# Kernel tuning notes

Measured on AMD Instinct MI355X. Metric: run time of the kernel, lower is better.

The kernel has to match this reference:

```python
import jax, jax.numpy as jnp
import numpy as np

T, B, SEQ_WIDTH, HID = 512, 64, 64, 1024
N = 32  # sqrt(HID): associative memory is N x N, HID spiking neurons
BETA = 0.9     # leak
THRESH = 1.0   # firing threshold
SLOPE = 25.0   # fast-sigmoid surrogate slope (snntorch default)


@jax.custom_vjp
def spike(u):
    # Heaviside forward, fast-sigmoid surrogate backward (snntorch-style)
    return (u > 0).astype(u.dtype)

def _spike_fwd(u):
    return (u > 0).astype(u.dtype), u

def _spike_bwd(u, g):
    sg = 1.0 / (1.0 + SLOPE * jnp.abs(u)) ** 2
    return (g * sg,)

spike.defvjp(_spike_fwd, _spike_bwd)


def assoc_leaky(h, Wk, bk, Wv, bv, Wq, bq):
    """Leaky associative spiking layer.
    h: (T, B, HID). Membrane state is an (B, N, N) associative matrix.
    Each step: outer-product write of key/value, leaky integration,
    threshold spike with soft reset, output spikes gated by sigmoid(q) rows.
    """
    k = h @ Wk + bk                      # (T, B, N)
    v = h @ Wv + bv                      # (T, B, N)
    q = jax.nn.sigmoid(h @ Wq + bq)      # (T, B, N)  use_q_projection gate
    Bt = h.shape[1]

    def step(mem, kvq):
        kt, vt, qt = kvq
        mem = BETA * mem + kt[:, :, None] * vt[:, None, :]   # (B, N, N)
        s = spike(mem - THRESH)
        mem = mem - s * THRESH                               # soft reset
        out = (s * qt[:, :, None]).reshape(Bt, N * N)        # (B, HID)
        return mem, out

    mem0 = jnp.zeros((Bt, N, N), h.dtype)
    _, outs = jax.lax.scan(step, mem0, (k, v, q))
    return outs  # (T, B, HID)


def setup_inputs() -> dict:
    key = jax.random.key(0)
    ks = jax.random.split(key, 12)
    s = 0.02
    def p(k, shape):
        return jax.random.normal(k, shape, jnp.float32) * s
    z = lambda *shape: jnp.zeros(shape, jnp.float32)
    return {
        "x": jax.random.normal(ks[0], (T, B, SEQ_WIDTH + 1), jnp.float32),
        "W_in": p(ks[1], (SEQ_WIDTH + 1, HID)), "b_in": z(HID),
        "Wk1": p(ks[2], (HID, N)), "bk1": z(N),
        "Wv1": p(ks[3], (HID, N)), "bv1": z(N),
        "Wq1": p(ks[4], (HID, N)), "bq1": z(N),
        "W_mid": p(ks[5], (HID, HID)), "b_mid": z(HID),
        "Wk2": p(ks[6], (HID, N)), "bk2": z(N),
        "Wv2": p(ks[7], (HID, N)), "bv2": z(N),
        "Wq2": p(ks[8], (HID, N)), "bq2": z(N),
        "W_out": p(ks[9], (HID, SEQ_WIDTH)), "b_out": z(SEQ_WIDTH),
    }


def reference(x, W_in, b_in, Wk1, bk1, Wv1, bv1, Wq1, bq1,
              W_mid, b_mid, Wk2, bk2, Wv2, bv2, Wq2, bq2, W_out, b_out):
    h = x @ W_in + b_in                                  # (T, B, HID)
    h = assoc_leaky(h, Wk1, bk1, Wv1, bv1, Wq1, bq1)
    h = jax.nn.relu(h @ W_mid + b_mid)
    h = assoc_leaky(h, Wk2, bk2, Wv2, bv2, Wq2, bq2)
    y = h @ W_out + b_out                                # (T, B, SEQ_WIDTH)
    return jax.nn.sigmoid(y)
```

## Files before the change

### kernel.cpp

```cpp
#include <hip/hip_runtime.h>
#include <math.h>


#define T_STEPS 512
#define BATCH   64
#define NN      32
#define HID     1024
#define INW     65
#define OUTW    64
#define KVQ     96

__device__ __forceinline__ float sigmoidf_(float x) { return 1.0f / (1.0f + expf(-x)); }

__global__ __launch_bounds__(512) void prep_kernel(
    const float* __restrict__ W_in, const float* __restrict__ b_in,
    const float* __restrict__ Wk1, const float* __restrict__ bk1,
    const float* __restrict__ Wv1, const float* __restrict__ bv1,
    const float* __restrict__ Wq1, const float* __restrict__ bq1,
    const float* __restrict__ b_mid,
    const float* __restrict__ Wk2, const float* __restrict__ bk2,
    const float* __restrict__ Wv2, const float* __restrict__ bv2,
    const float* __restrict__ Wq2, const float* __restrict__ bq2,
    float* __restrict__ W1eff, float* __restrict__ b1eff,
    float* __restrict__ const2)
{
    const int m = blockIdx.x;
    const int tid = threadIdx.x;
    __shared__ float srcv[HID];
    __shared__ float part[512];
    for (int h = tid; h < HID; h += 512) {
        float s;
        if (m < INW)       s = W_in[m * HID + h];
        else if (m == INW) s = b_in[h];
        else               s = fmaxf(b_mid[h], 0.f);
        srcv[h] = s;
    }
    __syncthreads();
    const int hq = tid >> 7, ns = tid & 127;
    const int sel = ns >> 5, nn = ns & 31;
    const bool layer2 = (m == INW + 1);
    const float* W = layer2 ? (sel == 0 ? Wk2 : sel == 1 ? Wv2 : Wq2)
                            : (sel == 0 ? Wk1 : sel == 1 ? Wv1 : Wq1);
    float acc = 0.f;
    if (ns < KVQ) {
        const int h0 = hq * 256;
        #pragma unroll 8
        for (int hh = 0; hh < 256; ++hh)
            acc = fmaf(srcv[h0 + hh], W[(h0 + hh) * NN + nn], acc);
    }
    part[tid] = acc;
    __syncthreads();
    if (hq == 0 && ns < KVQ) {
        float tot = part[ns] + part[128 + ns] + part[256 + ns] + part[384 + ns];
        if (m < INW) {
            W1eff[m * KVQ + ns] = tot;
        } else if (m == INW) {
            tot += (sel == 0 ? bk1 : sel == 1 ? bv1 : bq1)[nn];
            b1eff[ns] = tot;
        } else {
            tot += (sel == 0 ? bk2 : sel == 1 ? bv2 : bq2)[nn];
            const2[ns] = (sel == 2) ? sigmoidf_(tot) : tot;
        }
    }
}

__global__ __launch_bounds__(128) void kvq1p1_kernel(
    const float* __restrict__ x, const float* __restrict__ W1eff,
    const float* __restrict__ b1eff, float* __restrict__ kvq1,
    float* __restrict__ S, float* __restrict__ P)
{
    const int b = blockIdx.x >> 3, seg = blockIdx.x & 7;
    const int tid = threadIdx.x;
    __shared__ __align__(16) float Ws[INW * KVQ];
    __shared__ __align__(16) float bs[KVQ];
    __shared__ __align__(16) float pool[64 * 100];
    for (int i4 = tid; i4 < (INW * KVQ) / 4; i4 += 128)
        ((float4*)Ws)[i4] = ((const float4*)W1eff)[i4];
    if (tid < KVQ) bs[tid] = b1eff[tid];
    for (int l = tid; l < 64 * INW; l += 128) {
        const int r = l / INW, m = l - r * INW;
        pool[m * 68 + r] = x[((size_t)((seg * 64 + r) * 64 + b)) * INW + m];
    }
    __syncthreads();
    const int rg = tid >> 3;
    const int c0 = (tid & 7) * 12;
    float acc[4][12];
    #pragma unroll
    for (int r = 0; r < 4; ++r)
        #pragma unroll
        for (int k = 0; k < 12; ++k) acc[r][k] = bs[c0 + k];
    #pragma unroll 5
    for (int m = 0; m < INW; ++m) {
        const float4 xv = *(const float4*)&pool[m * 68 + rg * 4];
        const float4 w0 = *(const float4*)&Ws[m * KVQ + c0];
        const float4 w1 = *(const float4*)&Ws[m * KVQ + c0 + 4];
        const float4 w2 = *(const float4*)&Ws[m * KVQ + c0 + 8];
        const float xr[4] = {xv.x, xv.y, xv.z, xv.w};
        const float wk[12] = {w0.x, w0.y, w0.z, w0.w, w1.x, w1.y, w1.z, w1.w,
                              w2.x, w2.y, w2.z, w2.w};
        #pragma unroll
        for (int r = 0; r < 4; ++r)
            #pragma unroll
            for (int k = 0; k < 12; ++k)
                acc[r][k] = fmaf(xr[r], wk[k], acc[r][k]);
    }
    __syncthreads();
    #pragma unroll
    for (int r = 0; r < 4; ++r) {
        const int row = rg * 4 + r;
        float v[12];
        #pragma unroll
        for (int k = 0; k < 12; ++k)
            v[k] = (c0 + k >= 2 * NN) ? sigmoidf_(acc[r][k]) : acc[r][k];
        float* kt = &pool[row * 100 + c0];
        *(float4*)&kt[0] = make_float4(v[0], v[1], v[2], v[3]);
        *(float4*)&kt[4] = make_float4(v[4], v[5], v[6], v[7]);
        *(float4*)&kt[8] = make_float4(v[8], v[9], v[10], v[11]);
        float* o = kvq1 + ((size_t)b * T_STEPS + seg * 64 + row) * KVQ + c0;
        *(float4*)&o[0] = make_float4(v[0], v[1], v[2], v[3]);
        *(float4*)&o[4] = make_float4(v[4], v[5], v[6], v[7]);
        *(float4*)&o[8] = make_float4(v[8], v[9], v[10], v[11]);
    }
    __syncthreads();
    const int i0 = (tid >> 5) * 8, j = tid & 31;
    float p[8], am[8];
    #pragma unroll
    for (int r = 0; r < 8; ++r) { p[r] = 0.f; am[r] = 0.f; }
    for (int tt = 0; tt < 16; ++tt) {
        float4 k0[4], k1[4]; float vv[4];
        #pragma unroll
        for (int d2 = 0; d2 < 4; ++d2) {
            const int t = tt * 4 + d2;
            k0[d2] = *(const float4*)&pool[t * 100 + i0];
            k1[d2] = *(const float4*)&pool[t * 100 + i0 + 4];
            vv[d2] = pool[t * 100 + 32 + j];
        }
        #pragma unroll
        for (int d2 = 0; d2 < 4; ++d2) {
            const float kf[8] = {k0[d2].x, k0[d2].y, k0[d2].z, k0[d2].w,
                                 k1[d2].x, k1[d2].y, k1[d2].z, k1[d2].w};
            #pragma unroll
            for (int r = 0; r < 8; ++r) {
                p[r] = fmaf(0.9f, p[r], kf[r] * vv[d2]);
                am[r] = fmaxf(am[r], fabsf(p[r]));
            }
        }
    }
    const size_t o = ((size_t)seg * 64 + b) * 1024;
    #pragma unroll
    for (int r = 0; r < 8; ++r) {
        S[o + (i0 + r) * 32 + j] = p[r];
        P[o + (i0 + r) * 32 + j] = am[r];
    }
}

__global__ __launch_bounds__(256) void cc_kernel(
    const float* __restrict__ S, const float* __restrict__ P,
    const float* __restrict__ kvq,
    unsigned int* __restrict__ rowany, unsigned int* __restrict__ dmask)
{
    const int b = blockIdx.x;
    const int tid = threadIdx.x;
    const float c64 = 0.0011790184577738599f;
    float M[4] = {0.f, 0.f, 0.f, 0.f};
    bool fl = false;
    #pragma unroll
    for (int g = 0; g < 8; ++g) {
        #pragma unroll
        for (int k = 0; k < 4; ++k) {
            const size_t o = (size_t)g * 65536 + (size_t)b * 1024 + k * 256 + tid;
            const float s = S[o], pm = P[o];
            const float ub = fmaxf(M[k], 0.f) + pm;
            fl |= !(ub * 1.0001f <= 0.999f);
            M[k] = fmaf(c64, M[k], s);
        }
    }
    __shared__ unsigned int flr[4];
    const unsigned long long bal = __ballot(fl);
    if ((tid & 63) == 0) flr[tid >> 6] = (bal != 0ULL) ? 1u : 0u;
    __syncthreads();
    if ((flr[0] | flr[1] | flr[2] | flr[3]) == 0u) {
        if (tid < 64) rowany[b * 64 + tid] = 0u;
        return;
    }
    __shared__ float buf[64 * 64];
    const int j = tid & 31, ig = tid >> 5;
    const int wavei = tid >> 6;
    float mem[4] = {0.f, 0.f, 0.f, 0.f};
    unsigned int u[4] = {0u, 0u, 0u, 0u};
    for (int c = 0; c < 8; ++c) {
        __syncthreads();
        #pragma unroll
        for (int r = 0; r < 4; ++r) {
            const int s4 = tid + 256 * r;
            const int dt = s4 >> 4, q = s4 & 15;
            *(float4*)&buf[dt * 64 + q * 4] =
                *(const float4*)(kvq + ((size_t)b * T_STEPS + c * 64 + dt) * KVQ + q * 4);
        }
        __syncthreads();
        for (int dt = 0; dt < 64; ++dt) {
            const float4 kk = *(const float4*)&buf[dt * 64 + ig * 4];
            const float vv = buf[dt * 64 + 32 + j];
            const float kf[4] = {kk.x, kk.y, kk.z, kk.w};
            #pragma unroll
            for (int r = 0; r < 4; ++r) {
                mem[r] = fmaf(0.9f, mem[r], kf[r] * vv);
                const bool s = mem[r] > 1.f; if (s) mem[r] -= 1.f;
                u[r] |= (s ? 1u : 0u) << (dt & 31);
            }
            if ((dt & 31) == 31) {
                const int wg = c * 2 + (dt >> 5);
                unsigned int* dm = dmask + (size_t)(wg * 64 + b) * 1024;
                unsigned int a = 0;
                #pragma unroll
                for (int r = 0; r < 4; ++r) {
                    dm[(ig * 4 + r) * 32 + j] = u[r];
                    a |= u[r]; u[r] = 0u;
                }
                #pragma unroll
                for (int off = 32; off; off >>= 1) a |= __shfl_xor(a, off);
                if ((tid & 63) == 0) rowany[(b * 4 + wavei) * 16 + wg] = a;
            }
        }
    }
}

__global__ __launch_bounds__(128) void midp1_kernel(
    const unsigned int* __restrict__ rowany1, const unsigned int* __restrict__ dmask1,
    const float* __restrict__ kvq1,
    const float* __restrict__ W_mid, const float* __restrict__ b_mid,
    const float* __restrict__ Wk2, const float* __restrict__ bk2,
    const float* __restrict__ Wv2, const float* __restrict__ bv2,
    const float* __restrict__ Wq2, const float* __restrict__ bq2,
    const float* __restrict__ const2, float* __restrict__ kvq2,
    float* __restrict__ S2, float* __restrict__ P2)
{
    const int b = blockIdx.x >> 3, seg = blockIdx.x & 7;
    const int tid = threadIdx.x;
    const int w0 = seg * 2;
    const unsigned int orA = rowany1[(b * 4 + 0) * 16 + w0] | rowany1[(b * 4 + 1) * 16 + w0]
                           | rowany1[(b * 4 + 2) * 16 + w0] | rowany1[(b * 4 + 3) * 16 + w0];
    const unsigned int orB = rowany1[(b * 4 + 0) * 16 + w0 + 1] | rowany1[(b * 4 + 1) * 16 + w0 + 1]
                           | rowany1[(b * 4 + 2) * 16 + w0 + 1] | rowany1[(b * 4 + 3) * 16 + w0 + 1];
    __shared__ __align__(16) float c2s[KVQ];
    if (tid < KVQ) c2s[tid] = const2[tid];
    __syncthreads();
    float* obase = kvq2 + ((size_t)b * T_STEPS + seg * 64) * KVQ;
    const size_t o2 = ((size_t)seg * 64 + b) * 1024;
    const int i0 = (tid >> 5) * 8, j = tid & 31;
    const float G64 = 9.988209815422261f;
    if ((orA | orB) == 0u) {
        for (int l = tid; l < 64 * 24; l += 128) {
            const int row = l / 24, c4 = l - row * 24;
            *(float4*)&obase[row * KVQ + c4 * 4] = ((const float4*)c2s)[c4];
        }
        #pragma unroll
        for (int r = 0; r < 8; ++r) {
            const float s = c2s[i0 + r] * c2s[32 + j] * G64;
            S2[o2 + (i0 + r) * 32 + j] = s;
            P2[o2 + (i0 + r) * 32 + j] = fabsf(s);
        }
        return;
    }
    __shared__ __align__(16) float kt2[64 * 64];
    __shared__ float h2[HID];
    __shared__ unsigned int msk[NN];
    for (int d = 0; d < 64; ++d) {
        const unsigned int orw = (d < 32) ? orA : orB;
        const int bit = d & 31;
        if (!((orw >> bit) & 1u)) {
            if (tid < 16) *(float4*)&kt2[d * 64 + tid * 4] = ((const float4*)c2s)[tid];
            if (tid < 24) *(float4*)&obase[d * KVQ + tid * 4] = ((const float4*)c2s)[tid];
        } else {
            const int wg = w0 + (d >> 5);
            const unsigned int* dmw = dmask1 + (size_t)(wg * 64 + b) * 1024;
            for (int i2 = 0; i2 < NN; i2 += 4) {
                const int i = i2 + (tid >> 5);
                const unsigned int wb = dmw[i * 32 + (tid & 31)];
                const unsigned long long balm = __ballot(((wb >> bit) & 1u) != 0);
                const int ibase = i2 + (tid >> 6) * 2;
                if ((tid & 63) == 0)  msk[ibase]     = (unsigned int)balm;
                if ((tid & 63) == 32) msk[ibase + 1] = (unsigned int)(balm >> 32);
            }
            for (int cc = tid; cc < HID; cc += 128) h2[cc] = b_mid[cc];
            __syncthreads();
            const float* qrow = kvq1 + ((size_t)b * T_STEPS + seg * 64 + d) * KVQ + 2 * NN;
            for (int i = 0; i < NN; ++i) {
                unsigned int m = msk[i];
                if (!m) continue;
                const float qv = qrow[i];
                while (m) {
                    const int jj = __ffs(m) - 1; m &= m - 1;
                    const float* wr = W_mid + (size_t)(i * NN + jj) * HID;
                    for (int cc = tid; cc < HID; cc += 128)
                        h2[cc] = fmaf(qv, wr[cc], h2[cc]);
                }
            }
            __syncthreads();
            for (int cc = tid; cc < HID; cc += 128) h2[cc] = fmaxf(h2[cc], 0.f);
            __syncthreads();
            if (tid < KVQ) {
                const int sel = tid >> 5, nn = tid & 31;
                const float* W2 = sel == 0 ? Wk2 : sel == 1 ? Wv2 : Wq2;
                float a2 = (sel == 0 ? bk2 : sel == 1 ? bv2 : bq2)[nn];
                for (int cc = 0; cc < HID; ++cc)
                    a2 = fmaf(h2[cc], W2[cc * NN + nn], a2);
                if (sel == 2) a2 = sigmoidf_(a2);
                obase[d * KVQ + tid] = a2;
                if (tid < 64) kt2[d * 64 + tid] = a2;
            }
            __syncthreads();
        }
    }
    __syncthreads();
    float p[8], am[8];
    #pragma unroll
    for (int r = 0; r < 8; ++r) { p[r] = 0.f; am[r] = 0.f; }
    for (int tt = 0; tt < 16; ++tt) {
        float4 k0[4], k1[4]; float vv[4];
        #pragma unroll
        for (int d2 = 0; d2 < 4; ++d2) {
            const int t = tt * 4 + d2;
            k0[d2] = *(const float4*)&kt2[t * 64 + i0];
            k1[d2] = *(const float4*)&kt2[t * 64 + i0 + 4];
            vv[d2] = kt2[t * 64 + 32 + j];
        }
        #pragma unroll
        for (int d2 = 0; d2 < 4; ++d2) {
            const float kf[8] = {k0[d2].x, k0[d2].y, k0[d2].z, k0[d2].w,
                                 k1[d2].x, k1[d2].y, k1[d2].z, k1[d2].w};
            #pragma unroll
            for (int r = 0; r < 8; ++r) {
                p[r] = fmaf(0.9f, p[r], kf[r] * vv[d2]);
                am[r] = fmaxf(am[r], fabsf(p[r]));
            }
        }
    }
    #pragma unroll
    for (int r = 0; r < 8; ++r) {
        S2[o2 + (i0 + r) * 32 + j] = p[r];
        P2[o2 + (i0 + r) * 32 + j] = am[r];
    }
}

__global__ __launch_bounds__(256) void out_kernel(
    const unsigned int* __restrict__ rowany2, const unsigned int* __restrict__ dmask2,
    const float* __restrict__ kvq2,
    const float* __restrict__ W_out, const float* __restrict__ b_out,
    float* __restrict__ y)
{
    const int blk = blockIdx.x;
    const int b = blk >> 2, tq = blk & 3;
    const int tid = threadIdx.x;
    const int wave = tid >> 6, lane = tid & 63;
    const int wg = tq * 4 + wave;
    __shared__ unsigned int mskws[4][NN];
    const int g16 = lane & 15;
    const float4 bo = ((const float4*)b_out)[g16];
    const float4 sy = make_float4(sigmoidf_(bo.x), sigmoidf_(bo.y),
                                  sigmoidf_(bo.z), sigmoidf_(bo.w));
    const unsigned int or4 = rowany2[(b * 4 + 0) * 16 + wg]
                           | rowany2[(b * 4 + 1) * 16 + wg]
                           | rowany2[(b * 4 + 2) * 16 + wg]
                           | rowany2[(b * 4 + 3) * 16 + wg];
    if (or4 == 0) {
        #pragma unroll
        for (int d = 0; d < 32; d += 4) {
            const int t = wg * 32 + d + (lane >> 4);
            ((float4*)(y + ((size_t)t * 64 + b) * OUTW))[g16] = sy;
        }
        return;
    }
    for (int d = 0; d < 32; ++d) {
        const int t = wg * 32 + d;
        float* yr = y + ((size_t)t * 64 + b) * OUTW;
        if (!((or4 >> d) & 1u)) {
            if (lane < 16) ((float4*)yr)[lane] = sy;
            continue;
        }
        const unsigned int* dmw = dmask2 + (size_t)(wg * 64 + b) * 1024;
        for (int i2 = 0; i2 < NN; i2 += 2) {
            const int i = i2 + (lane >> 5), jj = lane & 31;
            const unsigned int wbits = dmw[i * 32 + jj];
            const unsigned long long bal = __ballot(((wbits >> d) & 1u) != 0);
            if (lane == 0)  mskws[wave][i2] = (unsigned int)bal;
            if (lane == 32) mskws[wave][i2 + 1] = (unsigned int)(bal >> 32);
        }
        const float* qrow = kvq2 + ((size_t)b * T_STEPS + t) * KVQ + 2 * NN;
        float a = b_out[lane];
        for (int i = 0; i < NN; ++i) {
            unsigned int m = mskws[wave][i];
            if (!m) continue;
            const float qv = qrow[i];
            while (m) {
                const int jj = __ffs(m) - 1; m &= m - 1;
                a = fmaf(qv, W_out[(size_t)(i * NN + jj) * OUTW + lane], a);
            }
        }
        yr[lane] = sigmoidf_(a);
    }
}

extern "C" void kernel_launch(void* const* d_in, const int* in_sizes, int n_in,
                              void* d_out, int out_size, void* d_ws, size_t ws_size,
                              hipStream_t stream)
{
    const float* x     = (const float*)d_in[0];
    const float* W_in  = (const float*)d_in[1];
    const float* b_in  = (const float*)d_in[2];
    const float* Wk1   = (const float*)d_in[3];
    const float* bk1   = (const float*)d_in[4];
    const float* Wv1   = (const float*)d_in[5];
    const float* bv1   = (const float*)d_in[6];
    const float* Wq1   = (const float*)d_in[7];
    const float* bq1   = (const float*)d_in[8];
    const float* W_mid = (const float*)d_in[9];
    const float* b_mid = (const float*)d_in[10];
    const float* Wk2   = (const float*)d_in[11];
    const float* bk2   = (const float*)d_in[12];
    const float* Wv2   = (const float*)d_in[13];
    const float* bv2   = (const float*)d_in[14];
    const float* Wq2   = (const float*)d_in[15];
    const float* bq2   = (const float*)d_in[16];
    const float* W_out = (const float*)d_in[17];
    const float* b_out = (const float*)d_in[18];
    float* y = (float*)d_out;

    float* ws = (float*)d_ws;
    float* W1eff  = ws;
    float* b1eff  = ws + 6240;
    float* const2 = ws + 6336;
    float* kvq1   = ws + 8192;
    float* kvq2   = kvq1 + 3145728;
    unsigned int* dmask1  = (unsigned int*)(kvq2 + 3145728);
    unsigned int* dmask2  = dmask1 + 1048576;
    unsigned int* rowany1 = dmask2 + 1048576;
    unsigned int* rowany2 = rowany1 + 4096;
    float* S1 = (float*)(rowany2 + 4096);
    float* P1 = S1 + 524288;
    float* S2 = P1 + 524288;
    float* P2 = S2 + 524288;

    prep_kernel<<<INW + 2, 512, 0, stream>>>(W_in, b_in, Wk1, bk1, Wv1, bv1, Wq1, bq1,
                                             b_mid, Wk2, bk2, Wv2, bv2, Wq2, bq2,
                                             W1eff, b1eff, const2);
    kvq1p1_kernel<<<BATCH * 8, 128, 0, stream>>>(x, W1eff, b1eff, kvq1, S1, P1);
    cc_kernel<<<BATCH, 256, 0, stream>>>(S1, P1, kvq1, rowany1, dmask1);
    midp1_kernel<<<BATCH * 8, 128, 0, stream>>>(rowany1, dmask1, kvq1, W_mid, b_mid,
                                                Wk2, bk2, Wv2, bv2, Wq2, bq2,
                                                const2, kvq2, S2, P2);
    cc_kernel<<<BATCH, 256, 0, stream>>>(S2, P2, kvq2, rowany2, dmask2);
    out_kernel<<<BATCH * 4, 256, 0, stream>>>(rowany2, dmask2, kvq2, W_out, b_out, y);
}
```

Measured before the change: 151.9 us.

## Replace per-element spike certificates with per-block max bounds and skip constant segments

```diff
diff --git a/kernel.cpp b/kernel.cpp
--- a/kernel.cpp
+++ b/kernel.cpp
@@ -67,13 +67,14 @@
 __global__ __launch_bounds__(128) void kvq1p1_kernel(
     const float* __restrict__ x, const float* __restrict__ W1eff,
     const float* __restrict__ b1eff, float* __restrict__ kvq1,
-    float* __restrict__ S, float* __restrict__ P)
+    float* __restrict__ cert1)
 {
     const int b = blockIdx.x >> 3, seg = blockIdx.x & 7;
     const int tid = threadIdx.x;
     __shared__ __align__(16) float Ws[INW * KVQ];
     __shared__ __align__(16) float bs[KVQ];
     __shared__ __align__(16) float pool[64 * 100];
+    __shared__ float red[4];
     for (int i4 = tid; i4 < (INW * KVQ) / 4; i4 += 128)
         ((float4*)Ws)[i4] = ((const float4*)W1eff)[i4];
     if (tid < KVQ) bs[tid] = b1eff[tid];
@@ -146,40 +147,66 @@
             }
         }
     }
-    const size_t o = ((size_t)seg * 64 + b) * 1024;
-    #pragma unroll
-    for (int r = 0; r < 8; ++r) {
-        S[o + (i0 + r) * 32 + j] = p[r];
-        P[o + (i0 + r) * 32 + j] = am[r];
+    float ls = 0.f, lp = 0.f;
+    #pragma unroll
+    for (int r = 0; r < 8; ++r) { ls = fmaxf(ls, fabsf(p[r])); lp = fmaxf(lp, am[r]); }
+    #pragma unroll
+    for (int off = 32; off; off >>= 1) {
+        ls = fmaxf(ls, __shfl_xor(ls, off));
+        lp = fmaxf(lp, __shfl_xor(lp, off));
+    }
+    const int lane = tid & 63, wv = tid >> 6;
+    if (lane == 0) { red[wv * 2] = ls; red[wv * 2 + 1] = lp; }
+    __syncthreads();
+    if (tid == 0) {
+        cert1[blockIdx.x * 2 + 0] = fmaxf(red[0], red[2]);
+        cert1[blockIdx.x * 2 + 1] = fmaxf(red[1], red[3]);
     }
 }
 
 __global__ __launch_bounds__(256) void cc_kernel(
-    const float* __restrict__ S, const float* __restrict__ P,
-    const float* __restrict__ kvq,
-    unsigned int* __restrict__ rowany, unsigned int* __restrict__ dmask)
+    const float* __restrict__ cert, const float* __restrict__ kvq,
+    unsigned int* __restrict__ rowany, unsigned int* __restrict__ dmask,
+    const unsigned int* __restrict__ rowany_prev, const float* __restrict__ cdef)
 {
     const int b = blockIdx.x;
     const int tid = threadIdx.x;
     const float c64 = 0.0011790184577738599f;
-    float M[4] = {0.f, 0.f, 0.f, 0.f};
+    const float G64 = 9.988209815422261f;
+    __shared__ __align__(16) float c2l[64];
+    float scs = 0.f;
+    if (cdef) {
+        if (tid < 64) c2l[tid] = cdef[tid];
+        __syncthreads();
+        float mk = 0.f, mv = 0.f;
+        #pragma unroll 8
+        for (int i = 0; i < 32; ++i) {
+            mk = fmaxf(mk, fabsf(c2l[i]));
+            mv = fmaxf(mv, fabsf(c2l[32 + i]));
+        }
+        scs = mk * mv * G64;
+    }
+    float Mb = 0.f;
     bool fl = false;
     #pragma unroll
     for (int g = 0; g < 8; ++g) {
-        #pragma unroll
-        for (int k = 0; k < 4; ++k) {
-            const size_t o = (size_t)g * 65536 + (size_t)b * 1024 + k * 256 + tid;
-            const float s = S[o], pm = P[o];
-            const float ub = fmaxf(M[k], 0.f) + pm;
-            fl |= !(ub * 1.0001f <= 0.999f);
-            M[k] = fmaf(c64, M[k], s);
-        }
-    }
-    __shared__ unsigned int flr[4];
-    const unsigned long long bal = __ballot(fl);
-    if ((tid & 63) == 0) flr[tid >> 6] = (bal != 0ULL) ? 1u : 0u;
-    __syncthreads();
-    if ((flr[0] | flr[1] | flr[2] | flr[3]) == 0u) {
+        bool mixed = true;
+        if (rowany_prev) {
+            unsigned int m = 0u;
+            #pragma unroll
+            for (int iq = 0; iq < 4; ++iq)
+                m |= rowany_prev[(b * 4 + iq) * 16 + 2 * g]
+                   | rowany_prev[(b * 4 + iq) * 16 + 2 * g + 1];
+            mixed = (m != 0u);
+        }
+        float smax, pmax;
+        if (mixed) { smax = cert[(b * 8 + g) * 2]; pmax = cert[(b * 8 + g) * 2 + 1]; }
+        else       { smax = scs; pmax = scs; }
+        const float ub = Mb + pmax;
+        fl |= !(ub * 1.0001f <= 0.999f);
+        Mb = fmaf(c64, Mb, smax);
+    }
+    if (!fl) {
         if (tid < 64) rowany[b * 64 + tid] = 0u;
         return;
     }
@@ -189,13 +216,27 @@
     float mem[4] = {0.f, 0.f, 0.f, 0.f};
     unsigned int u[4] = {0u, 0u, 0u, 0u};
     for (int c = 0; c < 8; ++c) {
+        unsigned int orA = 0xFFFFFFFFu, orB = 0xFFFFFFFFu;
+        if (rowany_prev) {
+            orA = 0u; orB = 0u;
+            #pragma unroll
+            for (int iq = 0; iq < 4; ++iq) {
+                orA |= rowany_prev[(b * 4 + iq) * 16 + 2 * c];
+                orB |= rowany_prev[(b * 4 + iq) * 16 + 2 * c + 1];
+            }
+        }
         __syncthreads();
         #pragma unroll
         for (int r = 0; r < 4; ++r) {
             const int s4 = tid + 256 * r;
             const int dt = s4 >> 4, q = s4 & 15;
-            *(float4*)&buf[dt * 64 + q * 4] =
-                *(const float4*)(kvq + ((size_t)b * T_STEPS + c * 64 + dt) * KVQ + q * 4);
+            const unsigned int orw = (dt < 32) ? orA : orB;
+            float4 val;
+            if (rowany_prev && !((orw >> (dt & 31)) & 1u))
+                val = *(const float4*)&c2l[q * 4];
+            else
+                val = *(const float4*)(kvq + ((size_t)b * T_STEPS + c * 64 + dt) * KVQ + q * 4);
+            *(float4*)&buf[dt * 64 + q * 4] = val;
         }
         __syncthreads();
         for (int dt = 0; dt < 64; ++dt) {
@@ -225,7 +266,7 @@
     }
 }
 
-__global__ __launch_bounds__(128) void midp1_kernel(
+__global__ __launch_bounds__(128) void mid_kernel(
     const unsigned int* __restrict__ rowany1, const unsigned int* __restrict__ dmask1,
     const float* __restrict__ kvq1,
     const float* __restrict__ W_mid, const float* __restrict__ b_mid,
@@ -233,7 +274,7 @@
     const float* __restrict__ Wv2, const float* __restrict__ bv2,
     const float* __restrict__ Wq2, const float* __restrict__ bq2,
     const float* __restrict__ const2, float* __restrict__ kvq2,
-    float* __restrict__ S2, float* __restrict__ P2)
+    float* __restrict__ cert2)
 {
     const int b = blockIdx.x >> 3, seg = blockIdx.x & 7;
     const int tid = threadIdx.x;
@@ -242,35 +283,20 @@
                            | rowany1[(b * 4 + 2) * 16 + w0] | rowany1[(b * 4 + 3) * 16 + w0];
     const unsigned int orB = rowany1[(b * 4 + 0) * 16 + w0 + 1] | rowany1[(b * 4 + 1) * 16 + w0 + 1]
                            | rowany1[(b * 4 + 2) * 16 + w0 + 1] | rowany1[(b * 4 + 3) * 16 + w0 + 1];
+    if ((orA | orB) == 0u) return;
     __shared__ __align__(16) float c2s[KVQ];
-    if (tid < KVQ) c2s[tid] = const2[tid];
-    __syncthreads();
-    float* obase = kvq2 + ((size_t)b * T_STEPS + seg * 64) * KVQ;
-    const size_t o2 = ((size_t)seg * 64 + b) * 1024;
-    const int i0 = (tid >> 5) * 8, j = tid & 31;
-    const float G64 = 9.988209815422261f;
-    if ((orA | orB) == 0u) {
-        for (int l = tid; l < 64 * 24; l += 128) {
-            const int row = l / 24, c4 = l - row * 24;
-            *(float4*)&obase[row * KVQ + c4 * 4] = ((const float4*)c2s)[c4];
-        }
-        #pragma unroll
-        for (int r = 0; r < 8; ++r) {
-            const float s = c2s[i0 + r] * c2s[32 + j] * G64;
-            S2[o2 + (i0 + r) * 32 + j] = s;
-            P2[o2 + (i0 + r) * 32 + j] = fabsf(s);
-        }
-        return;
-    }
     __shared__ __align__(16) float kt2[64 * 64];
     __shared__ float h2[HID];
     __shared__ unsigned int msk[NN];
+    __shared__ float red[4];
+    if (tid < KVQ) c2s[tid] = const2[tid];
+    __syncthreads();
+    float* obase = kvq2 + ((size_t)b * T_STEPS + seg * 64) * KVQ;
     for (int d = 0; d < 64; ++d) {
         const unsigned int orw = (d < 32) ? orA : orB;
         const int bit = d & 31;
         if (!((orw >> bit) & 1u)) {
             if (tid < 16) *(float4*)&kt2[d * 64 + tid * 4] = ((const float4*)c2s)[tid];
-            if (tid < 24) *(float4*)&obase[d * KVQ + tid * 4] = ((const float4*)c2s)[tid];
         } else {
             const int wg = w0 + (d >> 5);
             const unsigned int* dmw = dmask1 + (size_t)(wg * 64 + b) * 1024;
@@ -313,6 +339,7 @@
         }
     }
     __syncthreads();
+    const int i0 = (tid >> 5) * 8, j = tid & 31;
     float p[8], am[8];
     #pragma unroll
     for (int r = 0; r < 8; ++r) { p[r] = 0.f; am[r] = 0.f; }
@@ -336,16 +363,27 @@
             }
         }
     }
-    #pragma unroll
-    for (int r = 0; r < 8; ++r) {
-        S2[o2 + (i0 + r) * 32 + j] = p[r];
-        P2[o2 + (i0 + r) * 32 + j] = am[r];
+    float ls = 0.f, lp = 0.f;
+    #pragma unroll
+    for (int r = 0; r < 8; ++r) { ls = fmaxf(ls, fabsf(p[r])); lp = fmaxf(lp, am[r]); }
+    #pragma unroll
+    for (int off = 32; off; off >>= 1) {
+        ls = fmaxf(ls, __shfl_xor(ls, off));
+        lp = fmaxf(lp, __shfl_xor(lp, off));
+    }
+    const int lane = tid & 63, wv = tid >> 6;
+    if (lane == 0) { red[wv * 2] = ls; red[wv * 2 + 1] = lp; }
+    __syncthreads();
+    if (tid == 0) {
+        cert2[blockIdx.x * 2 + 0] = fmaxf(red[0], red[2]);
+        cert2[blockIdx.x * 2 + 1] = fmaxf(red[1], red[3]);
     }
 }
 
 __global__ __launch_bounds__(256) void out_kernel(
     const unsigned int* __restrict__ rowany2, const unsigned int* __restrict__ dmask2,
-    const float* __restrict__ kvq2,
+    const unsigned int* __restrict__ rowany1,
+    const float* __restrict__ kvq2, const float* __restrict__ const2,
     const float* __restrict__ W_out, const float* __restrict__ b_out,
     float* __restrict__ y)
 {
@@ -371,6 +409,10 @@
         }
         return;
     }
+    const unsigned int or1 = rowany1[(b * 4 + 0) * 16 + wg]
+                           | rowany1[(b * 4 + 1) * 16 + wg]
+                           | rowany1[(b * 4 + 2) * 16 + wg]
+                           | rowany1[(b * 4 + 3) * 16 + wg];
     for (int d = 0; d < 32; ++d) {
         const int t = wg * 32 + d;
         float* yr = y + ((size_t)t * 64 + b) * OUTW;
@@ -386,7 +428,9 @@
             if (lane == 0)  mskws[wave][i2] = (unsigned int)bal;
             if (lane == 32) mskws[wave][i2 + 1] = (unsigned int)(bal >> 32);
         }
-        const float* qrow = kvq2 + ((size_t)b * T_STEPS + t) * KVQ + 2 * NN;
+        const float* qrow = ((or1 >> d) & 1u)
+            ? kvq2 + ((size_t)b * T_STEPS + t) * KVQ + 2 * NN
+            : const2 + 2 * NN;
         float a = b_out[lane];
         for (int i = 0; i < NN; ++i) {
             unsigned int m = mskws[wave][i];
@@ -436,19 +480,21 @@
     unsigned int* dmask2  = dmask1 + 1048576;
     unsigned int* rowany1 = dmask2 + 1048576;
     unsigned int* rowany2 = rowany1 + 4096;
-    float* S1 = (float*)(rowany2 + 4096);
-    float* P1 = S1 + 524288;
-    float* S2 = P1 + 524288;
-    float* P2 = S2 + 524288;
+    float* cert1 = (float*)(rowany2 + 4096);
+    float* cert2 = cert1 + 1024;
 
     prep_kernel<<<INW + 2, 512, 0, stream>>>(W_in, b_in, Wk1, bk1, Wv1, bv1, Wq1, bq1,
                                              b_mid, Wk2, bk2, Wv2, bv2, Wq2, bq2,
                                              W1eff, b1eff, const2);
-    kvq1p1_kernel<<<BATCH * 8, 128, 0, stream>>>(x, W1eff, b1eff, kvq1, S1, P1);
-    cc_kernel<<<BATCH, 256, 0, stream>>>(S1, P1, kvq1, rowany1, dmask1);
-    midp1_kernel<<<BATCH * 8, 128, 0, stream>>>(rowany1, dmask1, kvq1, W_mid, b_mid,
-                                                Wk2, bk2, Wv2, bv2, Wq2, bq2,
-                                                const2, kvq2, S2, P2);
-    cc_kernel<<<BATCH, 256, 0, stream>>>(S2, P2, kvq2, rowany2, dmask2);
-    out_kernel<<<BATCH * 4, 256, 0, stream>>>(rowany2, dmask2, kvq2, W_out, b_out, y);
+    kvq1p1_kernel<<<BATCH * 8, 128, 0, stream>>>(x, W1eff, b1eff, kvq1, cert1);
+    cc_kernel<<<BATCH, 256, 0, stream>>>(cert1, kvq1, rowany1, dmask1,
+                                         (const unsigned int*)nullptr,
+                                         (const float*)nullptr);
+    mid_kernel<<<BATCH * 8, 128, 0, stream>>>(rowany1, dmask1, kvq1, W_mid, b_mid,
+                                              Wk2, bk2, Wv2, bv2, Wq2, bq2,
+                                              const2, kvq2, cert2);
+    cc_kernel<<<BATCH, 256, 0, stream>>>(cert2, kvq2, rowany2, dmask2,
+                                         rowany1, const2);
+    out_kernel<<<BATCH * 4, 256, 0, stream>>>(rowany2, dmask2, rowany1,
+                                              kvq2, const2, W_out, b_out, y);
 }
```

Result: faster. 147.6 us (-2.8%).
